# Kernel tuning notes

Measured on AMD Instinct MI355X. Metric: run time of the kernel, lower is better.

## Reference

```python
import jax, jax.numpy as jnp
import numpy as np
from jax import lax

K = 2000      # node_num of GraphConvolution
H, W = 75, 100  # edge_region_feature spatial grid (from per-pixel concat loops)


def setup_inputs() -> dict:
    key = jax.random.key(0)
    k1, k2, k3, k4 = jax.random.split(key, 4)
    b, c = 8, 512
    edge_region_feature = jax.random.normal(k1, (b, c, H, W), dtype=jnp.float32)
    edge_region_predict = jax.random.normal(k2, (b, 3, H, W), dtype=jnp.float32)
    # GraphConvolution params: kaiming_normal_(fan_out) weights, zero bias
    w1 = jax.random.normal(k3, (512, 128), dtype=jnp.float32) * np.sqrt(2.0 / 128)
    b1 = jnp.zeros((K, 128), dtype=jnp.float32)
    w2 = jax.random.normal(k4, (128, 128), dtype=jnp.float32) * np.sqrt(2.0 / 128)
    b2 = jnp.zeros((K, 128), dtype=jnp.float32)
    return {"edge_region_feature": edge_region_feature,
            "edge_region_predict": edge_region_predict,
            "w1": w1, "b1": b1, "w2": w2, "b2": b2}


def reference(edge_region_feature, edge_region_predict, w1, b1, w2, b2):
    b, c = edge_region_feature.shape[0], edge_region_feature.shape[1]
    # block_feature built as: for x in range(W) for y in range(H) -> node n at (y=n%H, x=n//H)
    block = jnp.transpose(edge_region_feature, (0, 3, 2, 1)).reshape(b, W * H, c)  # (b, 7500, 512)

    # topk over channel-0 prediction, flattened row-major (idx = y*W + x)
    scores = edge_region_predict[:, 0, :, :].reshape(b, -1)            # (b, 7500)
    _vals, topk_idx = lax.top_k(scores, K)
    sorted_idx = jnp.sort(topk_idx, axis=1)                            # (b, 2000) int32

    # gather node features (replicates original's indexing of block_feature)
    node_map = jnp.take_along_axis(block, sorted_idx[:, :, None], axis=1)  # (b, 2000, 512)

    # generate_adjacent_map: decode positions with width=W, connect 8-neighborhood (+self)
    py = sorted_idx // W
    px = sorted_idx % W
    near_y = jnp.abs(py[:, :, None] - py[:, None, :]) <= 1
    near_x = jnp.abs(px[:, :, None] - px[:, None, :]) <= 1
    adj = (near_y & near_x).astype(jnp.float32)                        # (b, 2000, 2000)

    # node_feature_grouping = ReLU6 -> GCN(512->128) -> GCN(128->128)
    inp = jnp.clip(jnp.concatenate([adj, node_map], axis=2), 0.0, 6.0)  # ReLU6 on cat(adj, nodes)
    a = inp[:, :, :K]
    nf = inp[:, :, K:]
    # GCN1: A @ X @ W1 + b1  (in!=out -> no residual)
    x1 = jnp.einsum('bij,bjf->bif', a, nf) @ w1 + b1                   # (b, 2000, 128)
    # GCN2: A @ X1 @ W2 + b2 + X1 (in==out -> residual)
    x2 = jnp.einsum('bij,bjf->bif', a, x1) @ w2 + b2 + x1              # (b, 2000, 128)

    node_output_feature = jnp.tanh(x2)
    return node_output_feature, sorted_idx
```

## Files before the change

kernel.cpp:

```cpp
#include <hip/hip_runtime.h>
#include <cmath>

#define H_DIM 75
#define W_DIM 100
#define HW 7500
#define KSEL 2000
#define BATCH 8
#define CIN 512
#define FDIM 128

typedef short v4s __attribute__((ext_vector_type(4)));
typedef short v8s __attribute__((ext_vector_type(8)));
typedef float v16f __attribute__((ext_vector_type(16)));

__device__ __forceinline__ unsigned int map_key(float f) {
  unsigned int u = __float_as_uint(f);
  return (u & 0x80000000u) ? ~u : (u | 0x80000000u);
}

__device__ __forceinline__ float fast_tanh(float x) {
  float e = __expf(2.0f * x);
  return 1.0f - 2.0f * __builtin_amdgcn_rcpf(e + 1.0f);
}

__device__ __forceinline__ unsigned short bf16_rne(float v) {
  unsigned int u = __float_as_uint(v);
  unsigned int r = u + 0x7FFFu + ((u >> 16) & 1u);
  return (unsigned short)(r >> 16);
}
__device__ __forceinline__ float bf16_to_f(unsigned short h) {
  return __uint_as_float(((unsigned int)h) << 16);
}

__global__ __launch_bounds__(1024) void topk_nbr_kernel(
    const float* __restrict__ pred, const float* __restrict__ w1,
    int* __restrict__ off_ws, float* __restrict__ out_idx,
    unsigned short* __restrict__ nbr, unsigned char* __restrict__ cnt,
    unsigned short* __restrict__ w1t_hi, unsigned short* __restrict__ w1t_lo)
{
  __shared__ unsigned int keys[HW];
  __shared__ unsigned int hist[256];
  __shared__ unsigned int partials[16];
  __shared__ unsigned int s_prefix, s_kth;
  const int tid = threadIdx.x;

  if (blockIdx.x >= BATCH) {
    int base = (blockIdx.x - BATCH) * 1024 + tid;
    #pragma unroll
    for (int e = base; e < CIN * FDIM; e += 8 * 1024) {
      int k = e & (CIN - 1), f = e >> 9;
      float v = w1[k * FDIM + f];
      unsigned short hi = bf16_rne(v);
      unsigned short lo = bf16_rne(v - bf16_to_f(hi));
      w1t_hi[(size_t)f * CIN + k] = hi;
      w1t_lo[(size_t)f * CIN + k] = lo;
    }
    return;
  }

  const int b = blockIdx.x;
  const int lane = tid & 63, w = tid >> 6;
  const float* scores = pred + (size_t)b * 3 * HW;
  for (int i = tid; i < HW; i += 1024) keys[i] = map_key(scores[i]);
  if (tid == 0) { s_prefix = 0u; s_kth = KSEL; }
  __syncthreads();

  for (int shift = 24; shift >= 0; shift -= 8) {
    if (tid < 256) hist[tid] = 0u;
    __syncthreads();
    unsigned int pref = s_prefix;
    unsigned int maskhi = (shift == 24) ? 0u : (0xFFFFFFFFu << (shift + 8));
    for (int i = tid; i < HW; i += 1024) {
      unsigned int k = keys[i];
      if ((k & maskhi) == pref) atomicAdd(&hist[(k >> shift) & 0xFFu], 1u);
    }
    __syncthreads();
    if (tid < 64) {
      unsigned int b0 = hist[tid * 4], b1 = hist[tid * 4 + 1];
      unsigned int b2 = hist[tid * 4 + 2], b3 = hist[tid * 4 + 3];
      unsigned int kth = s_kth;
      unsigned int T = b0 + b1 + b2 + b3;
      #pragma unroll
      for (int off = 1; off < 64; off <<= 1) {
        unsigned int t = __shfl_down(T, off, 64);
        if (tid + off < 64) T += t;
      }
      unsigned int U = __shfl_down(T, 1, 64);
      if (tid == 63) U = 0u;
      unsigned int s3 = b3 + U, s2 = b2 + s3, s1 = b1 + s2, s0 = b0 + s1;
      if (s0 >= kth && s1 < kth) { s_prefix = pref | ((unsigned)(4 * tid + 0) << shift); s_kth = kth - s1; }
      if (s1 >= kth && s2 < kth) { s_prefix = pref | ((unsigned)(4 * tid + 1) << shift); s_kth = kth - s2; }
      if (s2 >= kth && s3 < kth) { s_prefix = pref | ((unsigned)(4 * tid + 2) << shift); s_kth = kth - s3; }
      if (s3 >= kth && U  < kth) { s_prefix = pref | ((unsigned)(4 * tid + 3) << shift); s_kth = kth - U; }
    }
    __syncthreads();
  }
  const unsigned int thresh = s_prefix;

  unsigned int local[8];
  unsigned int sum = 0;
  #pragma unroll
  for (int e = 0; e < 8; ++e) {
    int i = tid * 8 + e;
    unsigned int p = 0;
    if (i < HW) {
      unsigned int ky = keys[i];
      if (ky > thresh) p = 1u;
      else if (ky == thresh) p = (1u << 16);
    }
    local[e] = p; sum += p;
  }
  __syncthreads();
  short* pos_of  = (short*)keys;
  int*   s_idx_sh = (int*)((char*)keys + 15000);
  for (int i = tid; i < HW; i += 1024) pos_of[i] = -1;

  unsigned int inc = sum;
  #pragma unroll
  for (int off = 1; off < 64; off <<= 1) {
    unsigned int t = __shfl_up(inc, off, 64);
    if (lane >= off) inc += t;
  }
  if (lane == 63) partials[w] = inc;
  __syncthreads();
  if (tid < 16) {
    unsigned int v = partials[tid];
    #pragma unroll
    for (int off = 1; off < 16; off <<= 1) {
      unsigned int t = __shfl_up(v, off, 64);
      if (tid >= off) v += t;
    }
    partials[tid] = v;
  }
  __syncthreads();
  unsigned int total = partials[15];
  unsigned int run = (w ? partials[w - 1] : 0u) + inc - sum;
  unsigned int ties = (unsigned int)KSEL - (total & 0xFFFFu);
  #pragma unroll
  for (int e = 0; e < 8; ++e) {
    int i = tid * 8 + e;
    unsigned int p = local[e];
    unsigned int gt_pref = run & 0xFFFFu;
    unsigned int eq_pref = run >> 16;
    bool sel = (p & 1u) || (((p >> 16) != 0u) && eq_pref < ties);
    if (sel) {
      unsigned int pos = gt_pref + (eq_pref < ties ? eq_pref : ties);
      off_ws[b * KSEL + pos] = (i % H_DIM) * W_DIM + i / H_DIM;
      out_idx[b * KSEL + pos] = (float)i;
      s_idx_sh[pos] = i;
      pos_of[i] = (short)pos;
    }
    run += p;
  }
  __syncthreads();

  for (int i = tid; i < KSEL; i += 1024) {
    int q = s_idx_sh[i];
    int py = q / W_DIM, px = q % W_DIM;
    unsigned short tmp[9];
    int c = 0;
    #pragma unroll
    for (int dy = -1; dy <= 1; ++dy) {
      int y = py + dy;
      if ((unsigned)y >= (unsigned)H_DIM) continue;
      #pragma unroll
      for (int dx = -1; dx <= 1; ++dx) {
        int x = px + dx;
        if ((unsigned)x >= (unsigned)W_DIM) continue;
        short p = pos_of[y * W_DIM + x];
        if (p >= 0) tmp[c++] = (unsigned short)p;
      }
    }
    #pragma unroll
    for (int t = 0; t < 9; ++t)
      nbr[(size_t)(b * KSEL + i) * 9 + t] = (t < c) ? tmp[t] : (unsigned short)0;
    cnt[b * KSEL + i] = (unsigned char)c;
  }
}

__global__ __launch_bounds__(512) void gather_kernel(
    const float* __restrict__ feat, const int* __restrict__ off_ws,
    unsigned short* __restrict__ nft_hi, unsigned short* __restrict__ nft_lo)
{
  __shared__ __align__(16) float s_plane[HW];
  const int b = blockIdx.y;
  const int c = blockIdx.x;
  const int tid = threadIdx.x;
  const float4* p4 = (const float4*)(feat + ((size_t)b * CIN + c) * HW);
  float4* sp4 = (float4*)s_plane;
  #pragma unroll
  for (int i = tid; i < HW / 4; i += 512)
    sp4[i] = p4[i];
  __syncthreads();
  if (tid < KSEL / 4) {
    const uint4* o4 = (const uint4*)off_ws + (size_t)b * (KSEL / 4);
    uint4 o = o4[tid];
    float v0 = fminf(fmaxf(s_plane[o.x], 0.f), 6.f);
    float v1 = fminf(fmaxf(s_plane[o.y], 0.f), 6.f);
    float v2 = fminf(fmaxf(s_plane[o.z], 0.f), 6.f);
    float v3 = fminf(fmaxf(s_plane[o.w], 0.f), 6.f);
    ushort4 h, l;
    h.x = bf16_rne(v0); l.x = bf16_rne(v0 - bf16_to_f(h.x));
    h.y = bf16_rne(v1); l.y = bf16_rne(v1 - bf16_to_f(h.y));
    h.z = bf16_rne(v2); l.z = bf16_rne(v2 - bf16_to_f(h.z));
    h.w = bf16_rne(v3); l.w = bf16_rne(v3 - bf16_to_f(h.w));
    size_t row = ((size_t)b * CIN + c) * KSEL;
    ((ushort4*)&nft_hi[row])[tid] = h;
    ((ushort4*)&nft_lo[row])[tid] = l;
  }
}

__global__ __launch_bounds__(256) void gemm1_mfma(
    const unsigned short* __restrict__ nft_hi,
    const unsigned short* __restrict__ nft_lo,
    const unsigned short* __restrict__ w1t_hi,
    const unsigned short* __restrict__ w1t_lo,
    float* __restrict__ G)
{
  __shared__ unsigned short a_hi[64][20], a_lo[64][20];
  __shared__ unsigned short b_hi[128][20], b_lo[128][20];
  const int b = blockIdx.y;
  const int n0 = blockIdx.x * 64;
  const int tid = threadIdx.x;
  const int lane = tid & 63, w = tid >> 6;
  const int wr = w & 1, wc = w >> 1;
  const int q = lane >> 5, m = lane & 31;
  v16f acc0, acc1;
  #pragma unroll
  for (int i = 0; i < 16; ++i) { acc0[i] = 0.f; acc1[i] = 0.f; }
  const unsigned short* nh = nft_hi + (size_t)b * CIN * KSEL;
  const unsigned short* nl = nft_lo + (size_t)b * CIN * KSEL;
  const int an = wr * 32 + m;
  const int f0 = wc * 64 + m;

  for (int k0 = 0; k0 < CIN; k0 += 16) {
    {
      int n = tid & 63, ks = (tid >> 6) * 4;
      #pragma unroll
      for (int j = 0; j < 4; ++j) {
        int k = ks + j;
        size_t gi = (size_t)(k0 + k) * KSEL + n0 + n;
        a_hi[n][k] = nh[gi];
        a_lo[n][k] = nl[gi];
      }
    }
    {
      int f = tid & 127, kh = tid >> 7;
      const ushort4* sh = (const ushort4*)&w1t_hi[(size_t)f * CIN + k0 + kh * 8];
      const ushort4* sl = (const ushort4*)&w1t_lo[(size_t)f * CIN + k0 + kh * 8];
      ushort4 h0 = sh[0], h1 = sh[1], l0 = sl[0], l1 = sl[1];
      *(ushort4*)&b_hi[f][kh * 8]     = h0;
      *(ushort4*)&b_hi[f][kh * 8 + 4] = h1;
      *(ushort4*)&b_lo[f][kh * 8]     = l0;
      *(ushort4*)&b_lo[f][kh * 8 + 4] = l1;
    }
    __syncthreads();
    v4s ah0 = *(const v4s*)&a_hi[an][q * 8];
    v4s ah1 = *(const v4s*)&a_hi[an][q * 8 + 4];
    v4s al0 = *(const v4s*)&a_lo[an][q * 8];
    v4s al1 = *(const v4s*)&a_lo[an][q * 8 + 4];
    v8s av_hi = __builtin_shufflevector(ah0, ah1, 0, 1, 2, 3, 4, 5, 6, 7);
    v8s av_lo = __builtin_shufflevector(al0, al1, 0, 1, 2, 3, 4, 5, 6, 7);
    {
      v4s bh0 = *(const v4s*)&b_hi[f0][q * 8];
      v4s bh1 = *(const v4s*)&b_hi[f0][q * 8 + 4];
      v4s bl0 = *(const v4s*)&b_lo[f0][q * 8];
      v4s bl1 = *(const v4s*)&b_lo[f0][q * 8 + 4];
      v8s bv_hi = __builtin_shufflevector(bh0, bh1, 0, 1, 2, 3, 4, 5, 6, 7);
      v8s bv_lo = __builtin_shufflevector(bl0, bl1, 0, 1, 2, 3, 4, 5, 6, 7);
      acc0 = __builtin_amdgcn_mfma_f32_32x32x16_bf16(av_hi, bv_hi, acc0, 0, 0, 0);
      acc0 = __builtin_amdgcn_mfma_f32_32x32x16_bf16(av_hi, bv_lo, acc0, 0, 0, 0);
      acc0 = __builtin_amdgcn_mfma_f32_32x32x16_bf16(av_lo, bv_hi, acc0, 0, 0, 0);
    }
    {
      v4s bh0 = *(const v4s*)&b_hi[f0 + 32][q * 8];
      v4s bh1 = *(const v4s*)&b_hi[f0 + 32][q * 8 + 4];
      v4s bl0 = *(const v4s*)&b_lo[f0 + 32][q * 8];
      v4s bl1 = *(const v4s*)&b_lo[f0 + 32][q * 8 + 4];
      v8s bv_hi = __builtin_shufflevector(bh0, bh1, 0, 1, 2, 3, 4, 5, 6, 7);
      v8s bv_lo = __builtin_shufflevector(bl0, bl1, 0, 1, 2, 3, 4, 5, 6, 7);
      acc1 = __builtin_amdgcn_mfma_f32_32x32x16_bf16(av_hi, bv_hi, acc1, 0, 0, 0);
      acc1 = __builtin_amdgcn_mfma_f32_32x32x16_bf16(av_hi, bv_lo, acc1, 0, 0, 0);
      acc1 = __builtin_amdgcn_mfma_f32_32x32x16_bf16(av_lo, bv_hi, acc1, 0, 0, 0);
    }
    __syncthreads();
  }
  float* ob = G + (size_t)b * KSEL * FDIM;
  #pragma unroll
  for (int reg = 0; reg < 16; ++reg) {
    int row = n0 + wr * 32 + (reg & 3) + 8 * (reg >> 2) + 4 * q;
    if (row < KSEL) {
      ob[(size_t)row * FDIM + f0]      = acc0[reg];
      ob[(size_t)row * FDIM + f0 + 32] = acc1[reg];
    }
  }
}

__global__ __launch_bounds__(256) void gemm2_kernel(
    const float* __restrict__ in, const float* __restrict__ wmat,
    float* __restrict__ out)
{
  __shared__ __align__(16) float a_lds[32][36];
  __shared__ __align__(16) float w_lds[32][128];
  const int b = blockIdx.y;
  const int n0 = blockIdx.x * 32;
  const int tid = threadIdx.x;
  const int tf = tid & 31, tr = tid >> 5;
  float acc[4][4] = {{0.f}};
  const float* fb = in + (size_t)b * KSEL * FDIM;
  for (int cc = 0; cc < FDIM; cc += 32) {
    const float4* w4 = (const float4*)(wmat + cc * 128);
    #pragma unroll
    for (int e = tid; e < 1024; e += 256) {
      int c = e >> 5, f4 = e & 31;
      ((float4*)&w_lds[c][0])[f4] = w4[e];
    }
    {
      int n = tid >> 3, c4 = tid & 7;
      float4 v = *(const float4*)&fb[(size_t)(n0 + n) * FDIM + cc + c4 * 4];
      a_lds[c4 * 4 + 0][n] = v.x;
      a_lds[c4 * 4 + 1][n] = v.y;
      a_lds[c4 * 4 + 2][n] = v.z;
      a_lds[c4 * 4 + 3][n] = v.w;
    }
    __syncthreads();
    #pragma unroll
    for (int c = 0; c < 32; ++c) {
      float4 av = *(const float4*)&a_lds[c][tr * 4];
      float4 wv = *(const float4*)&w_lds[c][tf * 4];
      acc[0][0] += av.x * wv.x; acc[0][1] += av.x * wv.y; acc[0][2] += av.x * wv.z; acc[0][3] += av.x * wv.w;
      acc[1][0] += av.y * wv.x; acc[1][1] += av.y * wv.y; acc[1][2] += av.y * wv.z; acc[1][3] += av.y * wv.w;
      acc[2][0] += av.z * wv.x; acc[2][1] += av.z * wv.y; acc[2][2] += av.z * wv.z; acc[2][3] += av.z * wv.w;
      acc[3][0] += av.w * wv.x; acc[3][1] += av.w * wv.y; acc[3][2] += av.w * wv.z; acc[3][3] += av.w * wv.w;
    }
    __syncthreads();
  }
  #pragma unroll
  for (int r = 0; r < 4; ++r) {
    int row = n0 + tr * 4 + r;
    if (row < KSEL) {
      float4 v = make_float4(acc[r][0], acc[r][1], acc[r][2], acc[r][3]);
      *(float4*)&out[((size_t)(b * KSEL + row)) * FDIM + tf * 4] = v;
    }
  }
}

__global__ __launch_bounds__(256) void x1_kernel(
    const float* __restrict__ G, const float* __restrict__ b1,
    const unsigned short* __restrict__ nbr, const unsigned char* __restrict__ cnt,
    float* __restrict__ x1)
{
  const int g = threadIdx.x >> 5, lane = threadIdx.x & 31;
  const int node = blockIdx.x * 8 + g;
  const int bb = blockIdx.y;
  const size_t bi = (size_t)bb * KSEL + node;
  const unsigned short* nb = nbr + bi * 9;
  unsigned short idx[9];
  #pragma unroll
  for (int t = 0; t < 9; ++t) idx[t] = nb[t];
  const int c = cnt[bi];
  const float4* G4 = (const float4*)G + (size_t)bb * KSEL * 32;
  float4 v[9];
  #pragma unroll
  for (int t = 0; t < 9; ++t) v[t] = G4[(size_t)idx[t] * 32 + lane];
  float4 acc = ((const float4*)b1)[node * 32 + lane];
  #pragma unroll
  for (int t = 0; t < 9; ++t) {
    float m = (t < c) ? 1.f : 0.f;
    acc.x = fmaf(v[t].x, m, acc.x);
    acc.y = fmaf(v[t].y, m, acc.y);
    acc.z = fmaf(v[t].z, m, acc.z);
    acc.w = fmaf(v[t].w, m, acc.w);
  }
  ((float4*)x1)[bi * 32 + lane] = acc;
}

__global__ __launch_bounds__(256) void out_kernel(
    const float* __restrict__ Hm, const float* __restrict__ x1,
    const float* __restrict__ b2,
    const unsigned short* __restrict__ nbr, const unsigned char* __restrict__ cnt,
    float* __restrict__ out)
{
  const int g = threadIdx.x >> 5, lane = threadIdx.x & 31;
  const int node = blockIdx.x * 8 + g;
  const int bb = blockIdx.y;
  const size_t bi = (size_t)bb * KSEL + node;
  const unsigned short* nb = nbr + bi * 9;
  unsigned short idx[9];
  #pragma unroll
  for (int t = 0; t < 9; ++t) idx[t] = nb[t];
  const int c = cnt[bi];
  const float4* H4 = (const float4*)Hm + (size_t)bb * KSEL * 32;
  float4 v[9];
  #pragma unroll
  for (int t = 0; t < 9; ++t) v[t] = H4[(size_t)idx[t] * 32 + lane];
  float4 acc = ((const float4*)b2)[node * 32 + lane];
  float4 xv = ((const float4*)x1)[bi * 32 + lane];
  acc.x += xv.x; acc.y += xv.y; acc.z += xv.z; acc.w += xv.w;
  #pragma unroll
  for (int t = 0; t < 9; ++t) {
    float m = (t < c) ? 1.f : 0.f;
    acc.x = fmaf(v[t].x, m, acc.x);
    acc.y = fmaf(v[t].y, m, acc.y);
    acc.z = fmaf(v[t].z, m, acc.z);
    acc.w = fmaf(v[t].w, m, acc.w);
  }
  float4 r;
  r.x = fast_tanh(acc.x); r.y = fast_tanh(acc.y);
  r.z = fast_tanh(acc.z); r.w = fast_tanh(acc.w);
  ((float4*)out)[bi * 32 + lane] = r;
}

extern "C" void kernel_launch(void* const* d_in, const int* in_sizes, int n_in,
                              void* d_out, int out_size, void* d_ws, size_t ws_size,
                              hipStream_t stream) {
  const float* feat = (const float*)d_in[0];
  const float* pred = (const float*)d_in[1];
  const float* w1   = (const float*)d_in[2];
  const float* b1   = (const float*)d_in[3];
  const float* w2   = (const float*)d_in[4];
  const float* b2   = (const float*)d_in[5];
  float* out0 = (float*)d_out;
  float* out_idx = out0 + (size_t)BATCH * KSEL * FDIM;

  char* ws = (char*)d_ws;
  int*            off_ws = (int*)(ws + 0);
  unsigned short* nbr    = (unsigned short*)(ws + 64256);
  unsigned char*  cnt    = (unsigned char*)(ws + 352512);
  float*          G      = (float*)(ws + 368640);
  char*           R      = ws + 8560640;
  unsigned short* nft_hi = (unsigned short*)R;
  unsigned short* nft_lo = (unsigned short*)(R + 16384000);
  unsigned short* w1t_hi = (unsigned short*)(R + 32768256);
  unsigned short* w1t_lo = (unsigned short*)(R + 32899328);
  float*          x1     = (float*)R;
  float*          Hm     = (float*)(R + 8388608);

  topk_nbr_kernel<<<BATCH + 8, 1024, 0, stream>>>(pred, w1, off_ws, out_idx,
                                                  nbr, cnt, w1t_hi, w1t_lo);
  gather_kernel<<<dim3(CIN, BATCH), 512, 0, stream>>>(feat, off_ws, nft_hi, nft_lo);
  gemm1_mfma<<<dim3(32, BATCH), 256, 0, stream>>>(nft_hi, nft_lo, w1t_hi, w1t_lo, G);
  x1_kernel<<<dim3(KSEL / 8, BATCH), 256, 0, stream>>>(G, b1, nbr, cnt, x1);
  gemm2_kernel<<<dim3(63, BATCH), 256, 0, stream>>>(x1, w2, Hm);
  out_kernel<<<dim3(KSEL / 8, BATCH), 256, 0, stream>>>(Hm, x1, b2, nbr, cnt, out0);
}
```

Baseline: 268.0 us.

## Move GEMM2 to split-bf16 MFMA, double-buffer GEMM1, privatize topk histograms

Replaces the scalar-FMA fp32 GEMM2 with an MFMA kernel using hi/lo bf16 splits of x1 and W2. x1_kernel now also writes the split x1, and the topk kernel pre-transposes and splits W2. GEMM1 now double-buffers its A tile in LDS and reads W1 fragments straight from global memory instead of staging them. The radix-select histogram uses per-wave private copies to cut atomic contention, at the cost of extra LDS and a reduction step.

```diff
diff --git a/kernel.cpp b/kernel.cpp
--- a/kernel.cpp
+++ b/kernel.cpp
@@ -34,11 +34,14 @@
 
 __global__ __launch_bounds__(1024) void topk_nbr_kernel(
     const float* __restrict__ pred, const float* __restrict__ w1,
+    const float* __restrict__ w2,
     int* __restrict__ off_ws, float* __restrict__ out_idx,
     unsigned short* __restrict__ nbr, unsigned char* __restrict__ cnt,
-    unsigned short* __restrict__ w1t_hi, unsigned short* __restrict__ w1t_lo)
+    unsigned short* __restrict__ w1t_hi, unsigned short* __restrict__ w1t_lo,
+    unsigned short* __restrict__ w2t_hi, unsigned short* __restrict__ w2t_lo)
 {
   __shared__ unsigned int keys[HW];
+  __shared__ unsigned int whist[16 * 256];
   __shared__ unsigned int hist[256];
   __shared__ unsigned int partials[16];
   __shared__ unsigned int s_prefix, s_kth;
@@ -46,14 +49,23 @@
 
   if (blockIdx.x >= BATCH) {
     int base = (blockIdx.x - BATCH) * 1024 + tid;
-    #pragma unroll
-    for (int e = base; e < CIN * FDIM; e += 8 * 1024) {
-      int k = e & (CIN - 1), f = e >> 9;
-      float v = w1[k * FDIM + f];
-      unsigned short hi = bf16_rne(v);
-      unsigned short lo = bf16_rne(v - bf16_to_f(hi));
-      w1t_hi[(size_t)f * CIN + k] = hi;
-      w1t_lo[(size_t)f * CIN + k] = lo;
+    for (int e = base; e < CIN * FDIM + FDIM * FDIM; e += 8 * 1024) {
+      if (e < CIN * FDIM) {
+        int k = e & (CIN - 1), f = e >> 9;
+        float v = w1[k * FDIM + f];
+        unsigned short hi = bf16_rne(v);
+        unsigned short lo = bf16_rne(v - bf16_to_f(hi));
+        w1t_hi[(size_t)f * CIN + k] = hi;
+        w1t_lo[(size_t)f * CIN + k] = lo;
+      } else {
+        int e2 = e - CIN * FDIM;
+        int k = e2 & (FDIM - 1), f = e2 >> 7;
+        float v = w2[k * FDIM + f];
+        unsigned short hi = bf16_rne(v);
+        unsigned short lo = bf16_rne(v - bf16_to_f(hi));
+        w2t_hi[(size_t)f * FDIM + k] = hi;
+        w2t_lo[(size_t)f * FDIM + k] = lo;
+      }
     }
     return;
   }
@@ -66,13 +78,21 @@
   __syncthreads();
 
   for (int shift = 24; shift >= 0; shift -= 8) {
-    if (tid < 256) hist[tid] = 0u;
+    for (int i = tid; i < 16 * 256; i += 1024) whist[i] = 0u;
     __syncthreads();
     unsigned int pref = s_prefix;
     unsigned int maskhi = (shift == 24) ? 0u : (0xFFFFFFFFu << (shift + 8));
     for (int i = tid; i < HW; i += 1024) {
       unsigned int k = keys[i];
-      if ((k & maskhi) == pref) atomicAdd(&hist[(k >> shift) & 0xFFu], 1u);
+      if ((k & maskhi) == pref)
+        atomicAdd(&whist[w * 256 + ((k >> shift) & 0xFFu)], 1u);
+    }
+    __syncthreads();
+    if (tid < 256) {
+      unsigned int s = 0;
+      #pragma unroll
+      for (int ww = 0; ww < 16; ++ww) s += whist[ww * 256 + tid];
+      hist[tid] = s;
     }
     __syncthreads();
     if (tid < 64) {
@@ -217,8 +237,7 @@
     const unsigned short* __restrict__ w1t_lo,
     float* __restrict__ G)
 {
-  __shared__ unsigned short a_hi[64][20], a_lo[64][20];
-  __shared__ unsigned short b_hi[128][20], b_lo[128][20];
+  __shared__ unsigned short a_hi[2][64][20], a_lo[2][64][20];
   const int b = blockIdx.y;
   const int n0 = blockIdx.x * 64;
   const int tid = threadIdx.x;
@@ -232,57 +251,42 @@
   const unsigned short* nl = nft_lo + (size_t)b * CIN * KSEL;
   const int an = wr * 32 + m;
   const int f0 = wc * 64 + m;
+  const int n_st = tid & 63, ks = (tid >> 6) * 4;
+
+  #pragma unroll
+  for (int j = 0; j < 4; ++j) {
+    size_t gi = (size_t)(ks + j) * KSEL + n0 + n_st;
+    a_hi[0][n_st][ks + j] = nh[gi];
+    a_lo[0][n_st][ks + j] = nl[gi];
+  }
+  __syncthreads();
 
   for (int k0 = 0; k0 < CIN; k0 += 16) {
-    {
-      int n = tid & 63, ks = (tid >> 6) * 4;
+    const int p = (k0 >> 4) & 1;
+    if (k0 + 16 < CIN) {
       #pragma unroll
       for (int j = 0; j < 4; ++j) {
-        int k = ks + j;
-        size_t gi = (size_t)(k0 + k) * KSEL + n0 + n;
-        a_hi[n][k] = nh[gi];
-        a_lo[n][k] = nl[gi];
+        size_t gi = (size_t)(k0 + 16 + ks + j) * KSEL + n0 + n_st;
+        a_hi[p ^ 1][n_st][ks + j] = nh[gi];
+        a_lo[p ^ 1][n_st][ks + j] = nl[gi];
       }
     }
-    {
-      int f = tid & 127, kh = tid >> 7;
-      const ushort4* sh = (const ushort4*)&w1t_hi[(size_t)f * CIN + k0 + kh * 8];
-      const ushort4* sl = (const ushort4*)&w1t_lo[(size_t)f * CIN + k0 + kh * 8];
-      ushort4 h0 = sh[0], h1 = sh[1], l0 = sl[0], l1 = sl[1];
-      *(ushort4*)&b_hi[f][kh * 8]     = h0;
-      *(ushort4*)&b_hi[f][kh * 8 + 4] = h1;
-      *(ushort4*)&b_lo[f][kh * 8]     = l0;
-      *(ushort4*)&b_lo[f][kh * 8 + 4] = l1;
-    }
-    __syncthreads();
-    v4s ah0 = *(const v4s*)&a_hi[an][q * 8];
-    v4s ah1 = *(const v4s*)&a_hi[an][q * 8 + 4];
-    v4s al0 = *(const v4s*)&a_lo[an][q * 8];
-    v4s al1 = *(const v4s*)&a_lo[an][q * 8 + 4];
-    v8s av_hi = __builtin_shufflevector(ah0, ah1, 0, 1, 2, 3, 4, 5, 6, 7);
-    v8s av_lo = __builtin_shufflevector(al0, al1, 0, 1, 2, 3, 4, 5, 6, 7);
-    {
-      v4s bh0 = *(const v4s*)&b_hi[f0][q * 8];
-      v4s bh1 = *(const v4s*)&b_hi[f0][q * 8 + 4];
-      v4s bl0 = *(const v4s*)&b_lo[f0][q * 8];
-      v4s bl1 = *(const v4s*)&b_lo[f0][q * 8 + 4];
-      v8s bv_hi = __builtin_shufflevector(bh0, bh1, 0, 1, 2, 3, 4, 5, 6, 7);
-      v8s bv_lo = __builtin_shufflevector(bl0, bl1, 0, 1, 2, 3, 4, 5, 6, 7);
-      acc0 = __builtin_amdgcn_mfma_f32_32x32x16_bf16(av_hi, bv_hi, acc0, 0, 0, 0);
-      acc0 = __builtin_amdgcn_mfma_f32_32x32x16_bf16(av_hi, bv_lo, acc0, 0, 0, 0);
-      acc0 = __builtin_amdgcn_mfma_f32_32x32x16_bf16(av_lo, bv_hi, acc0, 0, 0, 0);
-    }
-    {
-      v4s bh0 = *(const v4s*)&b_hi[f0 + 32][q * 8];
-      v4s bh1 = *(const v4s*)&b_hi[f0 + 32][q * 8 + 4];
-      v4s bl0 = *(const v4s*)&b_lo[f0 + 32][q * 8];
-      v4s bl1 = *(const v4s*)&b_lo[f0 + 32][q * 8 + 4];
-      v8s bv_hi = __builtin_shufflevector(bh0, bh1, 0, 1, 2, 3, 4, 5, 6, 7);
-      v8s bv_lo = __builtin_shufflevector(bl0, bl1, 0, 1, 2, 3, 4, 5, 6, 7);
-      acc1 = __builtin_amdgcn_mfma_f32_32x32x16_bf16(av_hi, bv_hi, acc1, 0, 0, 0);
-      acc1 = __builtin_amdgcn_mfma_f32_32x32x16_bf16(av_hi, bv_lo, acc1, 0, 0, 0);
-      acc1 = __builtin_amdgcn_mfma_f32_32x32x16_bf16(av_lo, bv_hi, acc1, 0, 0, 0);
-    }
+    v4s ah0 = *(const v4s*)&a_hi[p][an][q * 8];
+    v4s ah1 = *(const v4s*)&a_hi[p][an][q * 8 + 4];
+    v4s al0 = *(const v4s*)&a_lo[p][an][q * 8];
+    v4s al1 = *(const v4s*)&a_lo[p][an][q * 8 + 4];
+    v8s avh = __builtin_shufflevector(ah0, ah1, 0, 1, 2, 3, 4, 5, 6, 7);
+    v8s avl = __builtin_shufflevector(al0, al1, 0, 1, 2, 3, 4, 5, 6, 7);
+    v8s b0h = *(const v8s*)&w1t_hi[(size_t)f0 * CIN + k0 + q * 8];
+    v8s b0l = *(const v8s*)&w1t_lo[(size_t)f0 * CIN + k0 + q * 8];
+    v8s b1h = *(const v8s*)&w1t_hi[(size_t)(f0 + 32) * CIN + k0 + q * 8];
+    v8s b1l = *(const v8s*)&w1t_lo[(size_t)(f0 + 32) * CIN + k0 + q * 8];
+    acc0 = __builtin_amdgcn_mfma_f32_32x32x16_bf16(avh, b0h, acc0, 0, 0, 0);
+    acc0 = __builtin_amdgcn_mfma_f32_32x32x16_bf16(avh, b0l, acc0, 0, 0, 0);
+    acc0 = __builtin_amdgcn_mfma_f32_32x32x16_bf16(avl, b0h, acc0, 0, 0, 0);
+    acc1 = __builtin_amdgcn_mfma_f32_32x32x16_bf16(avh, b1h, acc1, 0, 0, 0);
+    acc1 = __builtin_amdgcn_mfma_f32_32x32x16_bf16(avh, b1l, acc1, 0, 0, 0);
+    acc1 = __builtin_amdgcn_mfma_f32_32x32x16_bf16(avl, b1h, acc1, 0, 0, 0);
     __syncthreads();
   }
   float* ob = G + (size_t)b * KSEL * FDIM;
@@ -296,59 +300,11 @@
   }
 }
 
-__global__ __launch_bounds__(256) void gemm2_kernel(
-    const float* __restrict__ in, const float* __restrict__ wmat,
-    float* __restrict__ out)
-{
-  __shared__ __align__(16) float a_lds[32][36];
-  __shared__ __align__(16) float w_lds[32][128];
-  const int b = blockIdx.y;
-  const int n0 = blockIdx.x * 32;
-  const int tid = threadIdx.x;
-  const int tf = tid & 31, tr = tid >> 5;
-  float acc[4][4] = {{0.f}};
-  const float* fb = in + (size_t)b * KSEL * FDIM;
-  for (int cc = 0; cc < FDIM; cc += 32) {
-    const float4* w4 = (const float4*)(wmat + cc * 128);
-    #pragma unroll
-    for (int e = tid; e < 1024; e += 256) {
-      int c = e >> 5, f4 = e & 31;
-      ((float4*)&w_lds[c][0])[f4] = w4[e];
-    }
-    {
-      int n = tid >> 3, c4 = tid & 7;
-      float4 v = *(const float4*)&fb[(size_t)(n0 + n) * FDIM + cc + c4 * 4];
-      a_lds[c4 * 4 + 0][n] = v.x;
-      a_lds[c4 * 4 + 1][n] = v.y;
-      a_lds[c4 * 4 + 2][n] = v.z;
-      a_lds[c4 * 4 + 3][n] = v.w;
-    }
-    __syncthreads();
-    #pragma unroll
-    for (int c = 0; c < 32; ++c) {
-      float4 av = *(const float4*)&a_lds[c][tr * 4];
-      float4 wv = *(const float4*)&w_lds[c][tf * 4];
-      acc[0][0] += av.x * wv.x; acc[0][1] += av.x * wv.y; acc[0][2] += av.x * wv.z; acc[0][3] += av.x * wv.w;
-      acc[1][0] += av.y * wv.x; acc[1][1] += av.y * wv.y; acc[1][2] += av.y * wv.z; acc[1][3] += av.y * wv.w;
-      acc[2][0] += av.z * wv.x; acc[2][1] += av.z * wv.y; acc[2][2] += av.z * wv.z; acc[2][3] += av.z * wv.w;
-      acc[3][0] += av.w * wv.x; acc[3][1] += av.w * wv.y; acc[3][2] += av.w * wv.z; acc[3][3] += av.w * wv.w;
-    }
-    __syncthreads();
-  }
-  #pragma unroll
-  for (int r = 0; r < 4; ++r) {
-    int row = n0 + tr * 4 + r;
-    if (row < KSEL) {
-      float4 v = make_float4(acc[r][0], acc[r][1], acc[r][2], acc[r][3]);
-      *(float4*)&out[((size_t)(b * KSEL + row)) * FDIM + tf * 4] = v;
-    }
-  }
-}
-
 __global__ __launch_bounds__(256) void x1_kernel(
     const float* __restrict__ G, const float* __restrict__ b1,
     const unsigned short* __restrict__ nbr, const unsigned char* __restrict__ cnt,
-    float* __restrict__ x1)
+    float* __restrict__ x1, unsigned short* __restrict__ x1h,
+    unsigned short* __restrict__ x1l)
 {
   const int g = threadIdx.x >> 5, lane = threadIdx.x & 31;
   const int node = blockIdx.x * 8 + g;
@@ -366,13 +322,67 @@
   float4 acc = ((const float4*)b1)[node * 32 + lane];
   #pragma unroll
   for (int t = 0; t < 9; ++t) {
-    float m = (t < c) ? 1.f : 0.f;
-    acc.x = fmaf(v[t].x, m, acc.x);
-    acc.y = fmaf(v[t].y, m, acc.y);
-    acc.z = fmaf(v[t].z, m, acc.z);
-    acc.w = fmaf(v[t].w, m, acc.w);
+    float mk = (t < c) ? 1.f : 0.f;
+    acc.x = fmaf(v[t].x, mk, acc.x);
+    acc.y = fmaf(v[t].y, mk, acc.y);
+    acc.z = fmaf(v[t].z, mk, acc.z);
+    acc.w = fmaf(v[t].w, mk, acc.w);
   }
   ((float4*)x1)[bi * 32 + lane] = acc;
+  ushort4 h, l;
+  h.x = bf16_rne(acc.x); l.x = bf16_rne(acc.x - bf16_to_f(h.x));
+  h.y = bf16_rne(acc.y); l.y = bf16_rne(acc.y - bf16_to_f(h.y));
+  h.z = bf16_rne(acc.z); l.z = bf16_rne(acc.z - bf16_to_f(h.z));
+  h.w = bf16_rne(acc.w); l.w = bf16_rne(acc.w - bf16_to_f(h.w));
+  ((ushort4*)x1h)[bi * 32 + lane] = h;
+  ((ushort4*)x1l)[bi * 32 + lane] = l;
+}
+
+__global__ __launch_bounds__(256) void gemm2_mfma(
+    const unsigned short* __restrict__ x1h,
+    const unsigned short* __restrict__ x1l,
+    const unsigned short* __restrict__ w2t_hi,
+    const unsigned short* __restrict__ w2t_lo,
+    float* __restrict__ Hm)
+{
+  const int b = blockIdx.y;
+  const int n0 = blockIdx.x * 64;
+  const int tid = threadIdx.x;
+  const int lane = tid & 63, w = tid >> 6;
+  const int wr = w & 1, wc = w >> 1;
+  const int q = lane >> 5, m = lane & 31;
+  int arow = n0 + wr * 32 + m;
+  if (arow > KSEL - 1) arow = KSEL - 1;
+  const unsigned short* xh = x1h + ((size_t)b * KSEL + arow) * FDIM;
+  const unsigned short* xl = x1l + ((size_t)b * KSEL + arow) * FDIM;
+  const int f0 = wc * 64 + m;
+  v16f acc0, acc1;
+  #pragma unroll
+  for (int i = 0; i < 16; ++i) { acc0[i] = 0.f; acc1[i] = 0.f; }
+  #pragma unroll
+  for (int k0 = 0; k0 < FDIM; k0 += 16) {
+    v8s avh = *(const v8s*)&xh[k0 + q * 8];
+    v8s avl = *(const v8s*)&xl[k0 + q * 8];
+    v8s b0h = *(const v8s*)&w2t_hi[(size_t)f0 * FDIM + k0 + q * 8];
+    v8s b0l = *(const v8s*)&w2t_lo[(size_t)f0 * FDIM + k0 + q * 8];
+    v8s b1h = *(const v8s*)&w2t_hi[(size_t)(f0 + 32) * FDIM + k0 + q * 8];
+    v8s b1l = *(const v8s*)&w2t_lo[(size_t)(f0 + 32) * FDIM + k0 + q * 8];
+    acc0 = __builtin_amdgcn_mfma_f32_32x32x16_bf16(avh, b0h, acc0, 0, 0, 0);
+    acc0 = __builtin_amdgcn_mfma_f32_32x32x16_bf16(avh, b0l, acc0, 0, 0, 0);
+    acc0 = __builtin_amdgcn_mfma_f32_32x32x16_bf16(avl, b0h, acc0, 0, 0, 0);
+    acc1 = __builtin_amdgcn_mfma_f32_32x32x16_bf16(avh, b1h, acc1, 0, 0, 0);
+    acc1 = __builtin_amdgcn_mfma_f32_32x32x16_bf16(avh, b1l, acc1, 0, 0, 0);
+    acc1 = __builtin_amdgcn_mfma_f32_32x32x16_bf16(avl, b1h, acc1, 0, 0, 0);
+  }
+  float* ob = Hm + (size_t)b * KSEL * FDIM;
+  #pragma unroll
+  for (int reg = 0; reg < 16; ++reg) {
+    int row = n0 + wr * 32 + (reg & 3) + 8 * (reg >> 2) + 4 * q;
+    if (row < KSEL) {
+      ob[(size_t)row * FDIM + f0]      = acc0[reg];
+      ob[(size_t)row * FDIM + f0 + 32] = acc1[reg];
+    }
+  }
 }
 
 __global__ __launch_bounds__(256) void out_kernel(
@@ -399,11 +409,11 @@
   acc.x += xv.x; acc.y += xv.y; acc.z += xv.z; acc.w += xv.w;
   #pragma unroll
   for (int t = 0; t < 9; ++t) {
-    float m = (t < c) ? 1.f : 0.f;
-    acc.x = fmaf(v[t].x, m, acc.x);
-    acc.y = fmaf(v[t].y, m, acc.y);
-    acc.z = fmaf(v[t].z, m, acc.z);
-    acc.w = fmaf(v[t].w, m, acc.w);
+    float mk = (t < c) ? 1.f : 0.f;
+    acc.x = fmaf(v[t].x, mk, acc.x);
+    acc.y = fmaf(v[t].y, mk, acc.y);
+    acc.z = fmaf(v[t].z, mk, acc.z);
+    acc.w = fmaf(v[t].w, mk, acc.w);
   }
   float4 r;
   r.x = fast_tanh(acc.x); r.y = fast_tanh(acc.y);
@@ -433,14 +443,18 @@
   unsigned short* nft_lo = (unsigned short*)(R + 16384000);
   unsigned short* w1t_hi = (unsigned short*)(R + 32768256);
   unsigned short* w1t_lo = (unsigned short*)(R + 32899328);
+  unsigned short* w2t_hi = (unsigned short*)(R + 33030656);
+  unsigned short* w2t_lo = (unsigned short*)(R + 33063424);
   float*          x1     = (float*)R;
   float*          Hm     = (float*)(R + 8388608);
-
-  topk_nbr_kernel<<<BATCH + 8, 1024, 0, stream>>>(pred, w1, off_ws, out_idx,
-                                                  nbr, cnt, w1t_hi, w1t_lo);
+  unsigned short* x1h    = (unsigned short*)(R + 16777216);
+  unsigned short* x1l    = (unsigned short*)(R + 20873472);
+
+  topk_nbr_kernel<<<BATCH + 8, 1024, 0, stream>>>(
+      pred, w1, w2, off_ws, out_idx, nbr, cnt, w1t_hi, w1t_lo, w2t_hi, w2t_lo);
   gather_kernel<<<dim3(CIN, BATCH), 512, 0, stream>>>(feat, off_ws, nft_hi, nft_lo);
   gemm1_mfma<<<dim3(32, BATCH), 256, 0, stream>>>(nft_hi, nft_lo, w1t_hi, w1t_lo, G);
-  x1_kernel<<<dim3(KSEL / 8, BATCH), 256, 0, stream>>>(G, b1, nbr, cnt, x1);
-  gemm2_kernel<<<dim3(63, BATCH), 256, 0, stream>>>(x1, w2, Hm);
+  x1_kernel<<<dim3(KSEL / 8, BATCH), 256, 0, stream>>>(G, b1, nbr, cnt, x1, x1h, x1l);
+  gemm2_mfma<<<dim3(32, BATCH), 256, 0, stream>>>(x1h, x1l, w2t_hi, w2t_lo, Hm);
   out_kernel<<<dim3(KSEL / 8, BATCH), 256, 0, stream>>>(Hm, x1, b2, nbr, cnt, out0);
 }
```

Result: faster. 262.0 us (-2.3%).
